# Kernel optimization log

Measured on AMD Instinct MI355X. Metric: run time of the kernel, lower is better.

## Reference

```python
import jax, jax.numpy as jnp
import numpy as np

N = 100_000      # num_nodes
E = 1_600_000    # num_edges (avg degree 16)
D = 64           # embedding_dim
L = 3            # num_layers


def setup_inputs() -> dict:
    key = jax.random.key(0)
    k1, k2 = jax.random.split(key)
    edge_index = jax.random.randint(k1, (2, E), 0, N, dtype=jnp.int64)
    edge_weight = jnp.ones((E,), jnp.float32)
    # nn.init.normal_(std=0.1)
    embedding = 0.1 * jax.random.normal(k2, (N, D), dtype=jnp.float32)
    return {"embedding": embedding, "edge_weight": edge_weight, "edge_index": edge_index}


def reference(embedding, edge_weight, edge_index):
    n = embedding.shape[0]
    self_idx = jnp.arange(n, dtype=edge_index.dtype)
    # add_self_loops: append (i, i) with weight 1 (PyG default fill_value)
    row = jnp.concatenate([edge_index[0], self_idx])  # source j
    col = jnp.concatenate([edge_index[1], self_idx])  # target i
    ew = jnp.concatenate([edge_weight, jnp.ones((n,), embedding.dtype)])
    # degree() counts occurrences of row (unweighted)
    deg = jax.ops.segment_sum(jnp.ones_like(ew), row, num_segments=n)
    deg_inv_sqrt = jnp.where(deg > 0, jax.lax.rsqrt(deg), 0.0)
    norm = deg_inv_sqrt[row] * ew * deg_inv_sqrt[col]  # [E+N]

    x = embedding
    acc = embedding  # running sum of layer-0..L embeddings
    for _ in range(L):
        # gather from source, scale, scatter-add to target (dropout off in eval)
        msg = norm[:, None] * x[row]                       # [E+N, D]
        x = jax.ops.segment_sum(msg, col, num_segments=n)  # [N, D]
        acc = acc + x
    return acc / (L + 1)
```

## Files before the change

### kernel.cpp

```cpp
#include <hip/hip_runtime.h>
#include <stdint.h>

#define DIM 64
#define GB 128
#define GSH 7
#define CH 8192
#define TB1 512
#define BINS2 50000
#define RANGES 2
#define NSLICE 64
#define TBH 1024

__device__ __forceinline__ unsigned bf16rne(float f) {
    unsigned u = __float_as_uint(f);
    return (u + 0x7FFFu + ((u >> 16) & 1u)) >> 16;
}
__device__ __forceinline__ unsigned pack2(float lo, float hi) {
    return bf16rne(lo) | (bf16rne(hi) << 16);
}
#define UNPK(u, lo, hi) { lo = __uint_as_float((u) << 16); hi = __uint_as_float((u) & 0xFFFF0000u); }

__global__ void __launch_bounds__(TBH)
hist_src_kernel(const int* __restrict__ src, const int* __restrict__ dst,
                unsigned short* __restrict__ partials, int* __restrict__ bcnt,
                int E, int N, int Es, int NB) {
    __shared__ unsigned h32[BINS2 / 2];
    __shared__ int hb[1024];
    const int b = blockIdx.x;
    const int r = b / NSLICE, s = b % NSLICE;
    const int base = r * BINS2;
    const int hi = min(base + BINS2, N);
    const int nbw = (hi - base + 1) >> 1;
    for (int j = threadIdx.x; j < nbw; j += TBH) h32[j] = 0;
    if (r == 0) for (int j = threadIdx.x; j < NB; j += TBH) hb[j] = 0;
    __syncthreads();
    const int e0 = s * Es, e1 = min(e0 + Es, E);
    if (r == 0) {
#pragma unroll 4
        for (int i = e0 + threadIdx.x; i < e1; i += TBH) {
            unsigned j = (unsigned)(src[i] - base);
            if (j < (unsigned)BINS2) atomicAdd(&h32[j >> 1], 1u << ((j & 1) * 16));
            atomicAdd(&hb[((unsigned)dst[i]) >> GSH], 1);
        }
    } else {
#pragma unroll 4
        for (int i = e0 + threadIdx.x; i < e1; i += TBH) {
            unsigned j = (unsigned)(src[i] - base);
            if (j < (unsigned)BINS2) atomicAdd(&h32[j >> 1], 1u << ((j & 1) * 16));
        }
    }
    __syncthreads();
    unsigned* part = (unsigned*)(partials + (size_t)s * N + base);
    for (int j = threadIdx.x; j < nbw; j += TBH) part[j] = h32[j];
    if (r == 0)
        for (int j = threadIdx.x; j < NB; j += TBH)
            if (hb[j]) atomicAdd(&bcnt[j], hb[j]);
}

__global__ void __launch_bounds__(256)
merge_dis_kernel(const unsigned short* __restrict__ partials, float* __restrict__ dis, int N) {
    const int i = blockIdx.x * blockDim.x + threadIdx.x;
    if (i >= N) return;
    int od = 0;
    for (int s = 0; s < NSLICE; ++s) od += partials[(size_t)s * N + i];
    dis[i] = rsqrtf((float)od + 1.0f);
}

__global__ void scan_buckets(const int* __restrict__ bcnt, int* __restrict__ bucket_base,
                             int* __restrict__ cursor, int* __restrict__ offsets,
                             int NB, int N) {
    __shared__ int buf[1024];
    const int t = threadIdx.x;
    int v = (t < NB) ? bcnt[t] : 0;
    buf[t] = v;
    __syncthreads();
    for (int off = 1; off < 1024; off <<= 1) {
        int add = (t >= off) ? buf[t - off] : 0;
        __syncthreads();
        buf[t] += add;
        __syncthreads();
    }
    if (t < NB) { bucket_base[t] = buf[t] - v; cursor[t] = buf[t] - v; }
    if (t == NB - 1) { bucket_base[NB] = buf[t]; offsets[N] = buf[t]; }
}

__global__ void __launch_bounds__(TB1)
part_kernel(const int* __restrict__ src, const int* __restrict__ dst,
            const float* __restrict__ ew, const float* __restrict__ dis,
            int* __restrict__ cursor, int2* __restrict__ staged, int E, int NB) {
    __shared__ int2 buf[CH];
    __shared__ int addr[CH];
    __shared__ int h[1024];
    __shared__ int sc[1024];
    __shared__ int gb[1024];
    const int tid = threadIdx.x;
    const int e0 = blockIdx.x * CH;
    const int e1 = min(e0 + CH, E);
    const int nrec = e1 - e0;
    for (int j = tid; j < 1024; j += TB1) h[j] = 0;
    __syncthreads();
    int4 d[4];
    int ngrp = 0;
    for (int i = e0 + tid * 4, k = 0; i < e1; i += TB1 * 4, ++k) {
        int4 t;
        if (i + 3 < e1) t = *(const int4*)(dst + i);
        else {
            t.x = dst[i];
            t.y = (i + 1 < e1) ? dst[i + 1] : -1;
            t.z = (i + 2 < e1) ? dst[i + 2] : -1;
            t.w = (i + 3 < e1) ? dst[i + 3] : -1;
        }
        d[k] = t;
        if (t.x >= 0) atomicAdd(&h[t.x >> GSH], 1);
        if (t.y >= 0) atomicAdd(&h[t.y >> GSH], 1);
        if (t.z >= 0) atomicAdd(&h[t.z >> GSH], 1);
        if (t.w >= 0) atomicAdd(&h[t.w >> GSH], 1);
        ngrp = k + 1;
    }
    __syncthreads();
    sc[tid] = h[tid]; sc[tid + 512] = h[tid + 512];
    __syncthreads();
    for (int off = 1; off < 1024; off <<= 1) {
        int a0 = (tid >= off) ? sc[tid - off] : 0;
        int a1 = sc[tid + 512 - off];
        __syncthreads();
        sc[tid] += a0; sc[tid + 512] += a1;
        __syncthreads();
    }
    for (int j = tid; j < NB; j += TB1) {
        int c = h[j];
        int ls = sc[j] - c;
        gb[j] = c ? atomicAdd(&cursor[j], c) : 0;
        h[j] = ls;
        sc[j] = ls;
    }
    __syncthreads();
    for (int i = e0 + tid * 4, k = 0; k < ngrp; i += TB1 * 4, ++k) {
        int4 t = d[k];
        int4 ss = make_int4(0, 0, 0, 0);
        float4 ww = make_float4(0.f, 0.f, 0.f, 0.f);
        if (i + 3 < e1) { ss = *(const int4*)(src + i); ww = *(const float4*)(ew + i); }
        else {
            ss.x = src[i]; ww.x = ew[i];
            if (i + 1 < e1) { ss.y = src[i + 1]; ww.y = ew[i + 1]; }
            if (i + 2 < e1) { ss.z = src[i + 2]; ww.z = ew[i + 2]; }
            if (i + 3 < e1) { ss.w = src[i + 3]; ww.w = ew[i + 3]; }
        }
#define PART1(T, S, W) if ((T) >= 0) { \
        int b_ = (T) >> GSH; \
        float w_ = dis[S] * (W) * dis[T]; \
        int lp_ = atomicAdd(&h[b_], 1); \
        buf[lp_] = make_int2((S) | (((T) & (GB - 1)) << 20), __float_as_int(w_)); \
        addr[lp_] = gb[b_] + (lp_ - sc[b_]); }
        PART1(t.x, ss.x, ww.x)
        PART1(t.y, ss.y, ww.y)
        PART1(t.z, ss.z, ww.z)
        PART1(t.w, ss.w, ww.w)
#undef PART1
    }
    __syncthreads();
    for (int k = tid; k < nrec; k += TB1)
        staged[addr[k]] = buf[k];
}

__global__ void __launch_bounds__(256)
place_kernel(const int2* __restrict__ staged, const int* __restrict__ bucket_base,
             int* __restrict__ offsets, int2* __restrict__ csr, int N) {
    __shared__ int cnt[GB];
    __shared__ int cur[GB];
    __shared__ int pre[GB + 1];
    const int b = blockIdx.x;
    const int n0 = b << GSH;
    const int nb = min(GB, N - n0);
    const int r0 = bucket_base[b], r1 = bucket_base[b + 1];
    for (int j = threadIdx.x; j < GB; j += 256) cnt[j] = 0;
    __syncthreads();
    for (int i = r0 + threadIdx.x; i < r1; i += 256)
        atomicAdd(&cnt[(staged[i].x >> 20) & (GB - 1)], 1);
    __syncthreads();
    if (threadIdx.x == 0) {
        int run = r0;
        for (int j = 0; j < nb; ++j) { pre[j] = run; run += cnt[j]; }
        pre[nb] = run;
    }
    __syncthreads();
    for (int j = threadIdx.x; j < nb; j += 256) { offsets[n0 + j] = pre[j]; cur[j] = pre[j]; }
    __syncthreads();
    for (int i = r0 + threadIdx.x; i < r1; i += 256) {
        int2 rec = staged[i];
        int tl = (rec.x >> 20) & (GB - 1);
        int rank = atomicAdd(&cur[tl], 1);
        csr[rank] = make_int2(rec.x & 0xFFFFF, rec.y);
    }
}

__global__ void __launch_bounds__(256)
conv_kernel(const float4* __restrict__ in4, uint4* __restrict__ outb, int n8) {
    int i = blockIdx.x * blockDim.x + threadIdx.x;
    if (i >= n8) return;
    float4 a = in4[2 * i], b = in4[2 * i + 1];
    uint4 o;
    o.x = pack2(a.x, a.y); o.y = pack2(a.z, a.w);
    o.z = pack2(b.x, b.y); o.w = pack2(b.z, b.w);
    outb[i] = o;
}

__global__ void __launch_bounds__(256)
prop_kernel(const uint4* __restrict__ xg, const float4* __restrict__ selfF,
            uint4* __restrict__ xstore,
            const int* __restrict__ offsets, const int2* __restrict__ csr,
            const float* __restrict__ dis, int n,
            const float4* __restrict__ embF, const uint4* __restrict__ xaF,
            float4* __restrict__ outF) {
    const int lane = threadIdx.x & 63;
    const int fl  = lane & 7;
    const int sub = lane >> 3;
    const int wave = blockIdx.x * (blockDim.x >> 6) + (threadIdx.x >> 6);
    const int node = wave * 8 + sub;
    if (node >= n) return;

    const int beg = offsets[node];
    const int end = offsets[node + 1];
    const float d = dis[node];
    const float dd = d * d;

    float a0, a1, a2, a3, a4, a5, a6, a7;
    uint4 qs = make_uint4(0, 0, 0, 0);
    if (selfF) {
        float4 s0 = selfF[(size_t)node * 16 + fl * 2];
        float4 s1 = selfF[(size_t)node * 16 + fl * 2 + 1];
        a0 = dd * s0.x; a1 = dd * s0.y; a2 = dd * s0.z; a3 = dd * s0.w;
        a4 = dd * s1.x; a5 = dd * s1.y; a6 = dd * s1.z; a7 = dd * s1.w;
    } else {
        qs = xg[(size_t)node * 8 + fl];
        float l, h;
        UNPK(qs.x, l, h) a0 = dd * l; a1 = dd * h;
        UNPK(qs.y, l, h) a2 = dd * l; a3 = dd * h;
        UNPK(qs.z, l, h) a4 = dd * l; a5 = dd * h;
        UNPK(qs.w, l, h) a6 = dd * l; a7 = dd * h;
    }

#define EDGE(E, Q) { float w_ = __int_as_float((E).y); float l, h; \
    UNPK((Q).x, l, h) a0 = fmaf(w_, l, a0); a1 = fmaf(w_, h, a1); \
    UNPK((Q).y, l, h) a2 = fmaf(w_, l, a2); a3 = fmaf(w_, h, a3); \
    UNPK((Q).z, l, h) a4 = fmaf(w_, l, a4); a5 = fmaf(w_, h, a5); \
    UNPK((Q).w, l, h) a6 = fmaf(w_, l, a6); a7 = fmaf(w_, h, a7); }

    int p = beg;
    for (; p + 8 <= end; p += 8) {
        int2 e0 = csr[p + 0], e1 = csr[p + 1], e2 = csr[p + 2], e3 = csr[p + 3];
        int2 e4 = csr[p + 4], e5 = csr[p + 5], e6 = csr[p + 6], e7 = csr[p + 7];
        uint4 q0 = xg[(size_t)e0.x * 8 + fl];
        uint4 q1 = xg[(size_t)e1.x * 8 + fl];
        uint4 q2 = xg[(size_t)e2.x * 8 + fl];
        uint4 q3 = xg[(size_t)e3.x * 8 + fl];
        uint4 q4 = xg[(size_t)e4.x * 8 + fl];
        uint4 q5 = xg[(size_t)e5.x * 8 + fl];
        uint4 q6 = xg[(size_t)e6.x * 8 + fl];
        uint4 q7 = xg[(size_t)e7.x * 8 + fl];
        EDGE(e0, q0) EDGE(e1, q1) EDGE(e2, q2) EDGE(e3, q3)
        EDGE(e4, q4) EDGE(e5, q5) EDGE(e6, q6) EDGE(e7, q7)
    }
    for (; p + 4 <= end; p += 4) {
        int2 e0 = csr[p + 0], e1 = csr[p + 1], e2 = csr[p + 2], e3 = csr[p + 3];
        uint4 q0 = xg[(size_t)e0.x * 8 + fl];
        uint4 q1 = xg[(size_t)e1.x * 8 + fl];
        uint4 q2 = xg[(size_t)e2.x * 8 + fl];
        uint4 q3 = xg[(size_t)e3.x * 8 + fl];
        EDGE(e0, q0) EDGE(e1, q1) EDGE(e2, q2) EDGE(e3, q3)
    }
    for (; p < end; ++p) {
        int2 e = csr[p];
        uint4 q = xg[(size_t)e.x * 8 + fl];
        EDGE(e, q)
    }
#undef EDGE

    if (outF) {
        float4 eA = embF[(size_t)node * 16 + fl * 2];
        float4 eB = embF[(size_t)node * 16 + fl * 2 + 1];
        uint4 qa = xaF[(size_t)node * 8 + fl];
        float r0 = eA.x + a0, r1 = eA.y + a1, r2 = eA.z + a2, r3 = eA.w + a3;
        float r4 = eB.x + a4, r5 = eB.y + a5, r6 = eB.z + a6, r7 = eB.w + a7;
        float l, h;
        UNPK(qa.x, l, h) r0 += l; r1 += h;
        UNPK(qa.y, l, h) r2 += l; r3 += h;
        UNPK(qa.z, l, h) r4 += l; r5 += h;
        UNPK(qa.w, l, h) r6 += l; r7 += h;
        UNPK(qs.x, l, h) r0 += l; r1 += h;
        UNPK(qs.y, l, h) r2 += l; r3 += h;
        UNPK(qs.z, l, h) r4 += l; r5 += h;
        UNPK(qs.w, l, h) r6 += l; r7 += h;
        outF[(size_t)node * 16 + fl * 2] =
            make_float4(0.25f * r0, 0.25f * r1, 0.25f * r2, 0.25f * r3);
        outF[(size_t)node * 16 + fl * 2 + 1] =
            make_float4(0.25f * r4, 0.25f * r5, 0.25f * r6, 0.25f * r7);
    } else {
        uint4 o;
        o.x = pack2(a0, a1); o.y = pack2(a2, a3);
        o.z = pack2(a4, a5); o.w = pack2(a6, a7);
        xstore[(size_t)node * 8 + fl] = o;
    }
}


extern "C" void kernel_launch(void* const* d_in, const int* in_sizes, int n_in,
                              void* d_out, int out_size, void* d_ws, size_t ws_size,
                              hipStream_t stream) {
    const float* emb = (const float*)d_in[0];
    const float* ew  = (const float*)d_in[1];
    const int*   ei  = (const int*)d_in[2];
    const int E = in_sizes[2] / 2;
    const int N = in_sizes[0] / DIM;
    const int* src = ei;
    const int* dst = ei + E;
    float* out = (float*)d_out;

    const int NB = (N + GB - 1) >> GSH;
    const int Es = (E + NSLICE - 1) / NSLICE;

    char* w = (char*)d_ws;
    size_t xSz = ((size_t)N * DIM * 2 + 255) & ~(size_t)255;
    size_t sSz = ((size_t)E * 8 + 255) & ~(size_t)255;
    size_t pSz = ((size_t)NSLICE * N * 2 + 255) & ~(size_t)255;
    size_t uSz = xSz > sSz ? xSz : sSz; if (pSz > uSz) uSz = pSz;
    unsigned short* partials = (unsigned short*)w;
    int2* staged = (int2*)w;
    uint4* xb    = (uint4*)w; w += uSz;
    int2* csr    = (int2*)w; w += sSz;
    uint4* x0c   = (uint4*)w; w += xSz;
    uint4* xa    = (uint4*)w; w += xSz;
    int* offsets = (int*)w; w += ((size_t)(N + 1) * 4 + 255) & ~(size_t)255;
    float* dis   = (float*)w; w += ((size_t)N * 4 + 255) & ~(size_t)255;
    int* bcnt        = (int*)w; w += 1024 * 4;
    int* bucket_base = (int*)w; w += 1025 * 4;
    int* cursor      = (int*)w; w += 1024 * 4;

    const int TB = 256;
    hipMemsetAsync(bcnt, 0, (size_t)NB * 4, stream);

    hist_src_kernel<<<RANGES * NSLICE, TBH, 0, stream>>>(src, dst, partials, bcnt,
                                                         E, N, Es, NB);
    merge_dis_kernel<<<(N + TB - 1) / TB, TB, 0, stream>>>(partials, dis, N);
    scan_buckets<<<1, 1024, 0, stream>>>(bcnt, bucket_base, cursor, offsets, NB, N);
    part_kernel<<<(E + CH - 1) / CH, TB1, 0, stream>>>(src, dst, ew, dis, cursor,
                                                       staged, E, NB);
    place_kernel<<<NB, TB, 0, stream>>>(staged, bucket_base, offsets, csr, N);

    const int n8 = N * DIM / 8;
    conv_kernel<<<(n8 + TB - 1) / TB, TB, 0, stream>>>((const float4*)emb, x0c, n8);

    dim3 grid((N + 31) / 32), block(TB);
    prop_kernel<<<grid, block, 0, stream>>>(x0c, (const float4*)emb, xa,
                                            offsets, csr, dis, N,
                                            nullptr, nullptr, nullptr);
    prop_kernel<<<grid, block, 0, stream>>>(xa, nullptr, xb,
                                            offsets, csr, dis, N,
                                            nullptr, nullptr, nullptr);
    prop_kernel<<<grid, block, 0, stream>>>(xb, nullptr, nullptr,
                                            offsets, csr, dis, N,
                                            (const float4*)emb, xa, (float4*)out);
}
```

Before: 282.1 us.

## Scatter partition records directly to global and defer normalization to place kernel

The partition kernel no longer stages records in shared memory or runs a block-wide scan. Each edge reserves its global slot through a shared atomic that holds the bucket's global cursor, then writes its record straight to the staged array. The symmetric normalization weight is now computed in the place kernel, which caches the target-side dis values for the bucket in shared memory. The chunk size is halved, giving more blocks with less shared memory each, in exchange for uncoalesced scattered global writes and more global cursor atomics.

```diff
diff --git a/kernel.cpp b/kernel.cpp
--- a/kernel.cpp
+++ b/kernel.cpp
@@ -4,7 +4,7 @@
 #define DIM 64
 #define GB 128
 #define GSH 7
-#define CH 8192
+#define CH 4096
 #define TB1 512
 #define BINS2 50000
 #define RANGES 2
@@ -86,20 +86,15 @@
 
 __global__ void __launch_bounds__(TB1)
 part_kernel(const int* __restrict__ src, const int* __restrict__ dst,
-            const float* __restrict__ ew, const float* __restrict__ dis,
+            const float* __restrict__ ew,
             int* __restrict__ cursor, int2* __restrict__ staged, int E, int NB) {
-    __shared__ int2 buf[CH];
-    __shared__ int addr[CH];
     __shared__ int h[1024];
-    __shared__ int sc[1024];
-    __shared__ int gb[1024];
     const int tid = threadIdx.x;
     const int e0 = blockIdx.x * CH;
     const int e1 = min(e0 + CH, E);
-    const int nrec = e1 - e0;
-    for (int j = tid; j < 1024; j += TB1) h[j] = 0;
-    __syncthreads();
-    int4 d[4];
+    for (int j = tid; j < NB; j += TB1) h[j] = 0;
+    __syncthreads();
+    int4 d[CH / (TB1 * 4)];
     int ngrp = 0;
     for (int i = e0 + tid * 4, k = 0; i < e1; i += TB1 * 4, ++k) {
         int4 t;
@@ -118,21 +113,9 @@
         ngrp = k + 1;
     }
     __syncthreads();
-    sc[tid] = h[tid]; sc[tid + 512] = h[tid + 512];
-    __syncthreads();
-    for (int off = 1; off < 1024; off <<= 1) {
-        int a0 = (tid >= off) ? sc[tid - off] : 0;
-        int a1 = sc[tid + 512 - off];
-        __syncthreads();
-        sc[tid] += a0; sc[tid + 512] += a1;
-        __syncthreads();
-    }
     for (int j = tid; j < NB; j += TB1) {
         int c = h[j];
-        int ls = sc[j] - c;
-        gb[j] = c ? atomicAdd(&cursor[j], c) : 0;
-        h[j] = ls;
-        sc[j] = ls;
+        h[j] = c ? atomicAdd(&cursor[j], c) : 0;
     }
     __syncthreads();
     for (int i = e0 + tid * 4, k = 0; k < ngrp; i += TB1 * 4, ++k) {
@@ -147,33 +130,30 @@
             if (i + 3 < e1) { ss.w = src[i + 3]; ww.w = ew[i + 3]; }
         }
 #define PART1(T, S, W) if ((T) >= 0) { \
-        int b_ = (T) >> GSH; \
-        float w_ = dis[S] * (W) * dis[T]; \
-        int lp_ = atomicAdd(&h[b_], 1); \
-        buf[lp_] = make_int2((S) | (((T) & (GB - 1)) << 20), __float_as_int(w_)); \
-        addr[lp_] = gb[b_] + (lp_ - sc[b_]); }
+        int pos_ = atomicAdd(&h[(T) >> GSH], 1); \
+        staged[pos_] = make_int2((S) | (((T) & (GB - 1)) << 20), __float_as_int(W)); }
         PART1(t.x, ss.x, ww.x)
         PART1(t.y, ss.y, ww.y)
         PART1(t.z, ss.z, ww.z)
         PART1(t.w, ss.w, ww.w)
 #undef PART1
     }
-    __syncthreads();
-    for (int k = tid; k < nrec; k += TB1)
-        staged[addr[k]] = buf[k];
 }
 
 __global__ void __launch_bounds__(256)
 place_kernel(const int2* __restrict__ staged, const int* __restrict__ bucket_base,
+             const float* __restrict__ dis,
              int* __restrict__ offsets, int2* __restrict__ csr, int N) {
     __shared__ int cnt[GB];
     __shared__ int cur[GB];
     __shared__ int pre[GB + 1];
+    __shared__ float disb[GB];
     const int b = blockIdx.x;
     const int n0 = b << GSH;
     const int nb = min(GB, N - n0);
     const int r0 = bucket_base[b], r1 = bucket_base[b + 1];
     for (int j = threadIdx.x; j < GB; j += 256) cnt[j] = 0;
+    for (int j = threadIdx.x; j < nb; j += 256) disb[j] = dis[n0 + j];
     __syncthreads();
     for (int i = r0 + threadIdx.x; i < r1; i += 256)
         atomicAdd(&cnt[(staged[i].x >> 20) & (GB - 1)], 1);
@@ -189,8 +169,10 @@
     for (int i = r0 + threadIdx.x; i < r1; i += 256) {
         int2 rec = staged[i];
         int tl = (rec.x >> 20) & (GB - 1);
+        int s = rec.x & 0xFFFFF;
         int rank = atomicAdd(&cur[tl], 1);
-        csr[rank] = make_int2(rec.x & 0xFFFFF, rec.y);
+        float w = dis[s] * __int_as_float(rec.y) * disb[tl];
+        csr[rank] = make_int2(s, __float_as_int(w));
     }
 }
 
@@ -343,9 +325,9 @@
                                                          E, N, Es, NB);
     merge_dis_kernel<<<(N + TB - 1) / TB, TB, 0, stream>>>(partials, dis, N);
     scan_buckets<<<1, 1024, 0, stream>>>(bcnt, bucket_base, cursor, offsets, NB, N);
-    part_kernel<<<(E + CH - 1) / CH, TB1, 0, stream>>>(src, dst, ew, dis, cursor,
+    part_kernel<<<(E + CH - 1) / CH, TB1, 0, stream>>>(src, dst, ew, cursor,
                                                        staged, E, NB);
-    place_kernel<<<NB, TB, 0, stream>>>(staged, bucket_base, offsets, csr, N);
+    place_kernel<<<NB, TB, 0, stream>>>(staged, bucket_base, dis, offsets, csr, N);
 
     const int n8 = N * DIM / 8;
     conv_kernel<<<(n8 + TB - 1) / TB, TB, 0, stream>>>((const float4*)emb, x0c, n8);
```

Result: faster. 270.2 us (-4.2%).
